# Optimization experiments

Hardware: AMD Instinct MI355X
Metric: run time of the kernel (lower is better)

The kernel has to match this reference:

```python
import jax, jax.numpy as jnp
import numpy as np

EPS = 1e-5

def _ln(x, g, b):
    mu = jnp.mean(x, axis=-1, keepdims=True)
    var = jnp.mean(jnp.square(x - mu), axis=-1, keepdims=True)
    return (x - mu) * jax.lax.rsqrt(var + EPS) * g + b

def setup_inputs() -> dict:
    key = jax.random.key(0)
    ks = jax.random.split(key, 16)
    B, L, D, H = 1, 512, 128, 128  # d_pair=128, d_hidden=128
    s_d = 1.0 / np.sqrt(D)
    s_h = 1.0 / np.sqrt(H)
    return {
        "pair": jax.random.normal(ks[0], (B, L, L, D), jnp.float32),
        "ln_g": jnp.ones((D,), jnp.float32),
        "ln_b": jnp.zeros((D,), jnp.float32),
        "lw": jax.random.normal(ks[1], (H, D), jnp.float32) * s_d,
        "lb": jnp.zeros((H,), jnp.float32),
        "lgw": jax.random.normal(ks[2], (H, D), jnp.float32) * s_d,
        "lgb": jnp.ones((H,), jnp.float32),
        "rw": jax.random.normal(ks[3], (H, D), jnp.float32) * s_d,
        "rb": jnp.zeros((H,), jnp.float32),
        "rgw": jax.random.normal(ks[4], (H, D), jnp.float32) * s_d,
        "rgb": jnp.ones((H,), jnp.float32),
        "gw": jax.random.normal(ks[5], (D, D), jnp.float32) * s_d,
        "gb": jnp.ones((D,), jnp.float32),
        "lno_g": jnp.ones((H,), jnp.float32),
        "lno_b": jnp.zeros((H,), jnp.float32),
        "ow": jax.random.normal(ks[6], (D, H), jnp.float32) * s_h,
        "ob": jnp.zeros((D,), jnp.float32),
    }

def reference(pair, ln_g, ln_b, lw, lb, lgw, lgb, rw, rb, rgw, rgb, gw, gb, lno_g, lno_b, ow, ob):
    L = pair.shape[1]
    p = _ln(pair, ln_g, ln_b)                                   # [B,L,L,D]
    left = jax.nn.sigmoid(p @ lgw.T + lgb) * (p @ lw.T + lb)    # [B,L,L,H]
    right = jax.nn.sigmoid(p @ rgw.T + rgb) * (p @ rw.T + rb)   # [B,L,L,H]
    # outgoing: contract over k (second seq dim)
    out = jnp.einsum('bikd,bjkd->bijd', left, right / jnp.float32(L))
    out = _ln(out, lno_g, lno_b)
    out = out @ ow.T + ob                                       # [B,L,L,D]
    gate = jax.nn.sigmoid(p @ gw.T + gb)
    return gate * out
```

## Files before the change

kernel.cpp:

```cpp
#include <hip/hip_runtime.h>
#include <hip/hip_bf16.h>
#include <stdint.h>

#define LSEQ 512
#define LL   262144

typedef __attribute__((ext_vector_type(8))) short short8;
typedef __attribute__((ext_vector_type(4))) float f32x4;
typedef __attribute__((ext_vector_type(4))) unsigned short us4;
typedef __attribute__((ext_vector_type(8))) unsigned short us8;

static_assert(sizeof(short8) == 16, "");
static_assert(sizeof(us8) == 16, "");

__device__ inline unsigned short f2bf(float f){
  unsigned u = __builtin_bit_cast(unsigned, f);
  unsigned r = (u + 0x7fffu + ((u >> 16) & 1u)) >> 16;
  return (unsigned short)r;
}
__device__ inline float bf2f(unsigned short s){
  return __builtin_bit_cast(float, ((unsigned)s) << 16);
}
__device__ inline float sigm(float x){ return 1.f / (1.f + __expf(-x)); }

__device__ inline int sw256(int row, int byte_in_row){
  return row*256 + ((((byte_in_row >> 4) ^ (row & 7))) << 4) + (byte_in_row & 15);
}
__device__ inline int sw128(int row, int byte_in_row){
  return row*128 + ((((byte_in_row >> 4) ^ (row & 7))) << 4) + (byte_in_row & 15);
}

__device__ inline void gload16(const void* g, void* lds){
  __builtin_amdgcn_global_load_lds(
      (const __attribute__((address_space(1))) unsigned*)g,
      (__attribute__((address_space(3))) unsigned*)lds, 16, 0, 0);
}

__global__ __launch_bounds__(128) void k0_prep(
    const float* __restrict__ ow, const float* __restrict__ lnog,
    const float* __restrict__ lnob, const float* __restrict__ ob,
    unsigned short* __restrict__ wgbf, float* __restrict__ swg, float* __restrict__ swb)
{
  const int dd = blockIdx.x;
  const int t  = threadIdx.x;
  const int idx = dd*128 + t;
  float o = ow[idx];
  float a = o * lnog[t];
  float b = o * lnob[t];
  wgbf[idx] = f2bf(a);
  #pragma unroll
  for (int m = 1; m < 64; m <<= 1){ a += __shfl_xor(a, m); b += __shfl_xor(b, m); }
  __shared__ float sA[2], sB[2];
  if ((t & 63) == 0){ sA[t >> 6] = a; sB[t >> 6] = b; }
  __syncthreads();
  if (t == 0){ swg[dd] = sA[0] + sA[1]; swb[dd] = sB[0] + sB[1] + ob[dd]; }
}

__global__ __launch_bounds__(64) void kP_pack(
    const float* __restrict__ lgw, const float* __restrict__ lw,
    const float* __restrict__ rgw, const float* __restrict__ rw,
    const float* __restrict__ gw, short8* __restrict__ wpk)
{
  const int b = blockIdx.x;
  const int arm = b >> 5, n = (b >> 2) & 7, ks = b & 3;
  const float* src = arm==0 ? lgw : arm==1 ? lw : arm==2 ? rgw : arm==3 ? rw : gw;
  const int l = threadIdx.x;
  const int h = n*16 + (l & 15), k0 = ks*32 + (l >> 4)*8;
  short8 v;
  #pragma unroll
  for (int e = 0; e < 8; ++e) v[e] = (short)f2bf(src[h*128 + k0 + e]);
  wpk[b*64 + l] = v;
}

__global__ __launch_bounds__(256, 3) void k1_proj(
    const float* __restrict__ pair, const float* __restrict__ ln_g, const float* __restrict__ ln_b,
    const float* __restrict__ lb,  const float* __restrict__ lgb,
    const float* __restrict__ rb,  const float* __restrict__ rgb,
    const float* __restrict__ gb,
    const short8* __restrict__ wpk,
    unsigned short* __restrict__ lt, unsigned short* __restrict__ rt,
    unsigned short* __restrict__ gate)
{
  __shared__ char p_l[16384];
  __shared__ char epi[16384];
  const int t = threadIdx.x;
  const int w = t >> 6, l = t & 63;
  const long pos0 = (long)blockIdx.x * 64;

  {
    const int col = (t & 31) * 4;
    const float4 g4 = *(const float4*)(ln_g + col);
    const float4 b4 = *(const float4*)(ln_b + col);
    #pragma unroll
    for (int pass = 0; pass < 8; ++pass){
      const int row = pass*8 + (t >> 5);
      const float4 x = *(const float4*)(pair + (pos0 + row)*128 + col);
      float s = x.x + x.y + x.z + x.w;
      float q = x.x*x.x + x.y*x.y + x.z*x.z + x.w*x.w;
      #pragma unroll
      for (int m = 1; m < 32; m <<= 1){ s += __shfl_xor(s, m); q += __shfl_xor(q, m); }
      const float mu = s * (1.f/128.f);
      const float rs = rsqrtf(q * (1.f/128.f) - mu*mu + 1e-5f);
      us4 o;
      o.x = f2bf((x.x - mu)*rs*g4.x + b4.x);
      o.y = f2bf((x.y - mu)*rs*g4.y + b4.y);
      o.z = f2bf((x.z - mu)*rs*g4.z + b4.z);
      o.w = f2bf((x.w - mu)*rs*g4.w + b4.w);
      *(us4*)(p_l + sw256(row, col*2)) = o;
    }
  }
  __syncthreads();

  short8 a[4][4];
  #pragma unroll
  for (int m = 0; m < 4; ++m)
    #pragma unroll
    for (int ks = 0; ks < 4; ++ks)
      a[m][ks] = *(const short8*)(p_l + sw256(m*16 + (l & 15), ks*64 + (l >> 4)*16));

  auto zero42 = [&](f32x4 (&acc)[4][2]){
    #pragma unroll
    for (int m = 0; m < 4; ++m){ acc[m][0] = f32x4{0,0,0,0}; acc[m][1] = f32x4{0,0,0,0}; }
  };

  auto gemm2 = [&](int armG, int armL, f32x4 (&aG)[4][2], f32x4 (&aL)[4][2]){
    #pragma unroll
    for (int n2 = 0; n2 < 2; ++n2){
      const int n = w*2 + n2;
      short8 bg[4], blv[4];
      #pragma unroll
      for (int ks = 0; ks < 4; ++ks){
        bg[ks]  = wpk[((armG*8 + n)*4 + ks)*64 + l];
        blv[ks] = wpk[((armL*8 + n)*4 + ks)*64 + l];
      }
      #pragma unroll
      for (int ks = 0; ks < 4; ++ks)
        #pragma unroll
        for (int m = 0; m < 4; ++m){
          aG[m][n2] = __builtin_amdgcn_mfma_f32_16x16x32_bf16(a[m][ks], bg[ks],  aG[m][n2], 0, 0, 0);
          aL[m][n2] = __builtin_amdgcn_mfma_f32_16x16x32_bf16(a[m][ks], blv[ks], aL[m][n2], 0, 0, 0);
        }
    }
  };

  auto epiT = [&](f32x4 (&aG)[4][2], f32x4 (&aL)[4][2],
                  const float* __restrict__ gbias, const float* __restrict__ lbias,
                  unsigned short* __restrict__ dst){
    #pragma unroll
    for (int n2 = 0; n2 < 2; ++n2){
      const int h = w*32 + n2*16 + (l & 15);
      const float gv = gbias[h], lv = lbias[h];
      #pragma unroll
      for (int m = 0; m < 4; ++m){
        us4 o;
        #pragma unroll
        for (int r = 0; r < 4; ++r)
          o[r] = f2bf(sigm(aG[m][n2][r] + gv) * (aL[m][n2][r] + lv));
        *(us4*)(epi + sw128(h, (m*16 + (l >> 4)*4)*2)) = o;
      }
    }
    __syncthreads();
    #pragma unroll
    for (int p = 0; p < 4; ++p){
      const int hh = p*32 + (t >> 3), ch = t & 7;
      us8 v = *(const us8*)(epi + sw128(hh, ch*16));
      *(us8*)(dst + (long)hh*LL + pos0 + ch*8) = v;
    }
    __syncthreads();
  };

  f32x4 aG[4][2], aL[4][2];

  zero42(aG); zero42(aL);
  gemm2(0, 1, aG, aL);
  epiT(aG, aL, lgb, lb, lt);

  zero42(aG); zero42(aL);
  gemm2(2, 3, aG, aL);
  epiT(aG, aL, rgb, rb, rt);

  zero42(aG);
  #pragma unroll
  for (int n2 = 0; n2 < 2; ++n2){
    const int n = w*2 + n2;
    short8 bg[4];
    #pragma unroll
    for (int ks = 0; ks < 4; ++ks) bg[ks] = wpk[((4*8 + n)*4 + ks)*64 + l];
    #pragma unroll
    for (int ks = 0; ks < 4; ++ks)
      #pragma unroll
      for (int m = 0; m < 4; ++m)
        aG[m][n2] = __builtin_amdgcn_mfma_f32_16x16x32_bf16(a[m][ks], bg[ks], aG[m][n2], 0, 0, 0);
  }
  {
    #pragma unroll
    for (int n2 = 0; n2 < 2; ++n2){
      const int h = w*32 + n2*16 + (l & 15);
      const float gv = gb[h];
      #pragma unroll
      for (int m = 0; m < 4; ++m)
        #pragma unroll
        for (int r = 0; r < 4; ++r){
          const int pos = m*16 + (l >> 4)*4 + r;
          *(unsigned short*)(epi + sw256(pos, h*2)) = f2bf(sigm(aG[m][n2][r] + gv));
        }
    }
    __syncthreads();
    #pragma unroll
    for (int p = 0; p < 4; ++p){
      const int row = p*16 + (t >> 4), ch = t & 15;
      us8 v = *(const us8*)(epi + sw256(row, ch*16));
      *(us8*)(gate + (pos0 + row)*128 + ch*8) = v;
    }
  }
}

__global__ __launch_bounds__(256) void k2_tri(
    const unsigned short* __restrict__ lt, const unsigned short* __restrict__ rt,
    unsigned short* __restrict__ omm)
{
  __shared__ char smem[32768];
  char* As = smem;
  char* Bs = smem + 16384;
  const int t = threadIdx.x, b = blockIdx.x;
  const int d = b & 127, tile = b >> 7;
  const int i0 = (tile >> 2)*128, j0 = (tile & 3)*128;
  const unsigned short* Ag = lt + (long)d*LL;
  const unsigned short* Bg = rt + (long)d*LL;
  const int w = t >> 6, l = t & 63;
  const int wm = w >> 1, wn = w & 1;

  f32x4 acc[4][4];
  #pragma unroll
  for (int m = 0; m < 4; ++m)
    #pragma unroll
    for (int n = 0; n < 4; ++n) acc[m][n] = f32x4{0.f,0.f,0.f,0.f};

  for (int kt = 0; kt < 8; ++kt){
    const int k0 = kt*64;
    __syncthreads();
    #pragma unroll
    for (int q = 0; q < 4; ++q){
      int P = q*4096 + t*16;
      int row = P >> 7;
      int ls  = ((P >> 4) & 7) ^ (row & 7);
      gload16(Ag + (long)(i0 + row)*512 + k0 + ls*8, As + P);
      gload16(Bg + (long)(j0 + row)*512 + k0 + ls*8, Bs + P);
    }
    __syncthreads();
    #pragma unroll
    for (int ks = 0; ks < 2; ++ks){
      short8 a[4], bb[4];
      #pragma unroll
      for (int m = 0; m < 4; ++m){
        int row = wm*64 + m*16 + (l & 15);
        a[m] = *(const short8*)(As + sw128(row, ks*64 + (l >> 4)*16));
      }
      #pragma unroll
      for (int n = 0; n < 4; ++n){
        int row = wn*64 + n*16 + (l & 15);
        bb[n] = *(const short8*)(Bs + sw128(row, ks*64 + (l >> 4)*16));
      }
      #pragma unroll
      for (int m = 0; m < 4; ++m)
        #pragma unroll
        for (int n = 0; n < 4; ++n)
          acc[m][n] = __builtin_amdgcn_mfma_f32_16x16x32_bf16(a[m], bb[n], acc[m][n], 0, 0, 0);
    }
  }
  __syncthreads();
  #pragma unroll
  for (int m = 0; m < 4; ++m)
    #pragma unroll
    for (int n = 0; n < 4; ++n)
      #pragma unroll
      for (int r = 0; r < 4; ++r){
        int row = wm*64 + m*16 + (l >> 4)*4 + r;
        int j   = wn*64 + n*16 + (l & 15);
        *(unsigned short*)(smem + sw256(row, j*2)) = f2bf(acc[m][n][r] * (1.f/512.f));
      }
  __syncthreads();
  #pragma unroll
  for (int it = 0; it < 8; ++it){
    int row = it*16 + (t >> 4), ch = t & 15;
    us8 v = *(const us8*)(smem + sw256(row, ch*16));
    *(us8*)(omm + (long)d*LL + (long)(i0 + row)*512 + j0 + ch*8) = v;
  }
}

__global__ __launch_bounds__(256) void k3_out(
    const unsigned short* __restrict__ omm, const unsigned short* __restrict__ gate,
    const unsigned short* __restrict__ wgbf,
    const float* __restrict__ swg, const float* __restrict__ swb,
    float* __restrict__ out)
{
  __shared__ char omm_l[32768];
  __shared__ char wg_l[32768];
  __shared__ float mu_s[128], rs_s[128];
  const int t = threadIdx.x;
  const int jt = blockIdx.x, i = blockIdx.y;
  const int j0 = jt*128;
  const int w = t >> 6, l = t & 63;

  {
    const int jc = t & 15, dg = t >> 4;
    float sum[8], sq[8];
    #pragma unroll
    for (int e = 0; e < 8; ++e){ sum[e] = 0.f; sq[e] = 0.f; }
    #pragma unroll
    for (int q = 0; q < 8; ++q){
      int dd = dg + q*16;
      us8 v = *(const us8*)(omm + (long)dd*LL + (long)i*512 + j0 + jc*8);
      *(us8*)(omm_l + dd*256 + jc*16) = v;
      #pragma unroll
      for (int e = 0; e < 8; ++e){
        float f = bf2f(v[e]);
        sum[e] += f; sq[e] += f*f;
      }
    }
    float* scr = (float*)wg_l;
    #pragma unroll
    for (int e = 0; e < 8; ++e){
      scr[dg*128 + jc*8 + e]        = sum[e];
      scr[2048 + dg*128 + jc*8 + e] = sq[e];
    }
  }
  __syncthreads();
  if (t < 128){
    const float* scr = (const float*)wg_l;
    float s1 = 0.f, s2 = 0.f;
    #pragma unroll
    for (int g = 0; g < 16; ++g){ s1 += scr[g*128 + t]; s2 += scr[2048 + g*128 + t]; }
    float mu = s1 * (1.f/128.f);
    float var = s2 * (1.f/128.f) - mu*mu;
    mu_s[t] = mu;
    rs_s[t] = rsqrtf(var + 1e-5f);
  }
  __syncthreads();
  #pragma unroll
  for (int q = 0; q < 8; ++q){
    int P = q*4096 + t*16;
    gload16((const char*)wgbf + sw256(P >> 8, P & 255), wg_l + P);
  }
  __syncthreads();

  f32x4 acc[2][8];
  #pragma unroll
  for (int m = 0; m < 2; ++m)
    #pragma unroll
    for (int n = 0; n < 8; ++n) acc[m][n] = f32x4{0.f,0.f,0.f,0.f};

  #pragma unroll
  for (int ks = 0; ks < 4; ++ks){
    short8 a[2];
    #pragma unroll
    for (int m = 0; m < 2; ++m){
      const int jj = w*32 + m*16 + (l & 15);
      short8 av;
      #pragma unroll
      for (int e = 0; e < 8; ++e){
        int dd = ks*32 + (l >> 4)*8 + e;
        av[e] = *(const short*)(omm_l + dd*256 + jj*2);
      }
      a[m] = av;
    }
    #pragma unroll
    for (int n = 0; n < 8; ++n){
      int row = n*16 + (l & 15);
      short8 bb = *(const short8*)(wg_l + sw256(row, ks*64 + (l >> 4)*16));
      #pragma unroll
      for (int m = 0; m < 2; ++m)
        acc[m][n] = __builtin_amdgcn_mfma_f32_16x16x32_bf16(a[m], bb, acc[m][n], 0, 0, 0);
    }
  }

  float swgv[8], swbv[8];
  #pragma unroll
  for (int n = 0; n < 8; ++n){ swgv[n] = swg[n*16 + (l & 15)]; swbv[n] = swb[n*16 + (l & 15)]; }
  #pragma unroll
  for (int m = 0; m < 2; ++m){
    #pragma unroll
    for (int r = 0; r < 4; ++r){
      int j = w*32 + m*16 + (l >> 4)*4 + r;
      float mu = mu_s[j], rs = rs_s[j];
      long rowoff = ((long)i*512 + j0 + j)*128;
      #pragma unroll
      for (int n = 0; n < 8; ++n){
        int ddx = n*16 + (l & 15);
        float val = rs*(acc[m][n][r] - mu*swgv[n]) + swbv[n];
        out[rowoff + ddx] = val * bf2f(gate[rowoff + ddx]);
      }
    }
  }
}

extern "C" void kernel_launch(void* const* d_in, const int* in_sizes, int n_in,
                              void* d_out, int out_size, void* d_ws, size_t ws_size,
                              hipStream_t stream)
{
  const float* pair = (const float*)d_in[0];
  const float* ln_g = (const float*)d_in[1];
  const float* ln_b = (const float*)d_in[2];
  const float* lw   = (const float*)d_in[3];
  const float* lb   = (const float*)d_in[4];
  const float* lgw  = (const float*)d_in[5];
  const float* lgb  = (const float*)d_in[6];
  const float* rw   = (const float*)d_in[7];
  const float* rb   = (const float*)d_in[8];
  const float* rgw  = (const float*)d_in[9];
  const float* rgb  = (const float*)d_in[10];
  const float* gw   = (const float*)d_in[11];
  const float* gb   = (const float*)d_in[12];
  const float* lnog = (const float*)d_in[13];
  const float* lnob = (const float*)d_in[14];
  const float* ow   = (const float*)d_in[15];
  const float* ob   = (const float*)d_in[16];
  float* out = (float*)d_out;

  char* ws = (char*)d_ws;
  unsigned short* lt   = (unsigned short*)(ws);
  unsigned short* rt   = (unsigned short*)(ws + (1l << 26));
  unsigned short* gate = (unsigned short*)(ws + (2l << 26));
  unsigned short* omm  = (unsigned short*)(ws + (3l << 26));
  short8*         wpk  = (short8*)(ws + (3l << 26));
  unsigned short* wgbf = (unsigned short*)(ws + (4l << 26));
  float* swg = (float*)(ws + (4l << 26) + 65536);
  float* swb = swg + 128;

  k0_prep<<<dim3(128), dim3(128), 0, stream>>>(ow, lnog, lnob, ob, wgbf, swg, swb);
  kP_pack<<<dim3(160), dim3(64), 0, stream>>>(lgw, lw, rgw, rw, gw, wpk);
  k1_proj<<<dim3(4096), dim3(256), 0, stream>>>(pair, ln_g, ln_b, lb, lgb, rb, rgb, gb,
                                                wpk, lt, rt, gate);
  k2_tri<<<dim3(2048), dim3(256), 0, stream>>>(lt, rt, omm);
  k3_out<<<dim3(4, 512), dim3(256), 0, stream>>>(omm, gate, wgbf, swg, swb, out);
}
```

Measured before the change: 297.9 us.

## Cut k1 LDS and registers, write lt/rt directly, remap k2 block order

The projection kernel drops its second 16KB LDS epilogue buffer and the preloaded A-fragment register array. It now reloads A fragments from LDS per k-step and writes the transposed lt/rt outputs straight from the MFMA accumulators as 8-byte stores, which removes two barriers per arm. Launch bounds rise to 4 blocks per CU, and the LayerNorm prologue loads four float4 per thread with a shorter shuffle reduction. The triangle kernel remaps block indices so consecutive blocks share the same d channel, probably to spread work across XCDs and reuse lt/rt in L2. The cost is more LDS reads and less coalesced global stores for lt/rt.

```diff
diff --git a/kernel.cpp b/kernel.cpp
--- a/kernel.cpp
+++ b/kernel.cpp
@@ -72,7 +72,7 @@
   wpk[b*64 + l] = v;
 }
 
-__global__ __launch_bounds__(256, 3) void k1_proj(
+__global__ __launch_bounds__(256, 4) void k1_proj(
     const float* __restrict__ pair, const float* __restrict__ ln_g, const float* __restrict__ ln_b,
     const float* __restrict__ lb,  const float* __restrict__ lgb,
     const float* __restrict__ rb,  const float* __restrict__ rgb,
@@ -82,70 +82,75 @@
     unsigned short* __restrict__ gate)
 {
   __shared__ char p_l[16384];
-  __shared__ char epi[16384];
   const int t = threadIdx.x;
   const int w = t >> 6, l = t & 63;
   const long pos0 = (long)blockIdx.x * 64;
 
   {
-    const int col = (t & 31) * 4;
-    const float4 g4 = *(const float4*)(ln_g + col);
-    const float4 b4 = *(const float4*)(ln_b + col);
-    #pragma unroll
-    for (int pass = 0; pass < 8; ++pass){
-      const int row = pass*8 + (t >> 5);
-      const float4 x = *(const float4*)(pair + (pos0 + row)*128 + col);
-      float s = x.x + x.y + x.z + x.w;
-      float q = x.x*x.x + x.y*x.y + x.z*x.z + x.w*x.w;
-      #pragma unroll
-      for (int m = 1; m < 32; m <<= 1){ s += __shfl_xor(s, m); q += __shfl_xor(q, m); }
+    const int q8 = t & 7;
+    float4 g4[4], b4[4];
+    #pragma unroll
+    for (int i = 0; i < 4; ++i){
+      g4[i] = *(const float4*)(ln_g + q8*4 + i*32);
+      b4[i] = *(const float4*)(ln_b + q8*4 + i*32);
+    }
+    #pragma unroll
+    for (int pass = 0; pass < 2; ++pass){
+      const int row = pass*32 + (t >> 3);
+      float4 x[4];
+      #pragma unroll
+      for (int i = 0; i < 4; ++i)
+        x[i] = *(const float4*)(pair + (pos0 + row)*128 + q8*4 + i*32);
+      float s = 0.f, qq = 0.f;
+      #pragma unroll
+      for (int i = 0; i < 4; ++i){
+        s  += (x[i].x + x[i].y) + (x[i].z + x[i].w);
+        qq += (x[i].x*x[i].x + x[i].y*x[i].y) + (x[i].z*x[i].z + x[i].w*x[i].w);
+      }
+      #pragma unroll
+      for (int msk = 1; msk < 8; msk <<= 1){ s += __shfl_xor(s, msk); qq += __shfl_xor(qq, msk); }
       const float mu = s * (1.f/128.f);
-      const float rs = rsqrtf(q * (1.f/128.f) - mu*mu + 1e-5f);
-      us4 o;
-      o.x = f2bf((x.x - mu)*rs*g4.x + b4.x);
-      o.y = f2bf((x.y - mu)*rs*g4.y + b4.y);
-      o.z = f2bf((x.z - mu)*rs*g4.z + b4.z);
-      o.w = f2bf((x.w - mu)*rs*g4.w + b4.w);
-      *(us4*)(p_l + sw256(row, col*2)) = o;
-    }
-  }
-  __syncthreads();
-
-  short8 a[4][4];
-  #pragma unroll
-  for (int m = 0; m < 4; ++m)
-    #pragma unroll
-    for (int ks = 0; ks < 4; ++ks)
-      a[m][ks] = *(const short8*)(p_l + sw256(m*16 + (l & 15), ks*64 + (l >> 4)*16));
-
-  auto zero42 = [&](f32x4 (&acc)[4][2]){
+      const float rs = rsqrtf(qq * (1.f/128.f) - mu*mu + 1e-5f);
+      #pragma unroll
+      for (int i = 0; i < 4; ++i){
+        us4 o;
+        o.x = f2bf((x[i].x - mu)*rs*g4[i].x + b4[i].x);
+        o.y = f2bf((x[i].y - mu)*rs*g4[i].y + b4[i].y);
+        o.z = f2bf((x[i].z - mu)*rs*g4[i].z + b4[i].z);
+        o.w = f2bf((x[i].w - mu)*rs*g4[i].w + b4[i].w);
+        *(us4*)(p_l + sw256(row, q8*8 + i*64)) = o;
+      }
+    }
+  }
+  __syncthreads();
+
+  f32x4 aG[4][2], aL[4][2];
+  auto zero = [&](f32x4 (&acc)[4][2]){
     #pragma unroll
     for (int m = 0; m < 4; ++m){ acc[m][0] = f32x4{0,0,0,0}; acc[m][1] = f32x4{0,0,0,0}; }
   };
-
-  auto gemm2 = [&](int armG, int armL, f32x4 (&aG)[4][2], f32x4 (&aL)[4][2]){
-    #pragma unroll
-    for (int n2 = 0; n2 < 2; ++n2){
-      const int n = w*2 + n2;
-      short8 bg[4], blv[4];
-      #pragma unroll
-      for (int ks = 0; ks < 4; ++ks){
-        bg[ks]  = wpk[((armG*8 + n)*4 + ks)*64 + l];
-        blv[ks] = wpk[((armL*8 + n)*4 + ks)*64 + l];
-      }
-      #pragma unroll
-      for (int ks = 0; ks < 4; ++ks)
+  auto gemm2 = [&](int armG, int armL){
+    #pragma unroll
+    for (int ks = 0; ks < 4; ++ks){
+      short8 av[4];
+      #pragma unroll
+      for (int m = 0; m < 4; ++m)
+        av[m] = *(const short8*)(p_l + sw256(m*16 + (l & 15), ks*64 + (l >> 4)*16));
+      #pragma unroll
+      for (int n2 = 0; n2 < 2; ++n2){
+        const int n = w*2 + n2;
+        const short8 bg = wpk[((armG*8 + n)*4 + ks)*64 + l];
+        const short8 bl = wpk[((armL*8 + n)*4 + ks)*64 + l];
         #pragma unroll
         for (int m = 0; m < 4; ++m){
-          aG[m][n2] = __builtin_amdgcn_mfma_f32_16x16x32_bf16(a[m][ks], bg[ks],  aG[m][n2], 0, 0, 0);
-          aL[m][n2] = __builtin_amdgcn_mfma_f32_16x16x32_bf16(a[m][ks], blv[ks], aL[m][n2], 0, 0, 0);
+          aG[m][n2] = __builtin_amdgcn_mfma_f32_16x16x32_bf16(av[m], bg, aG[m][n2], 0, 0, 0);
+          aL[m][n2] = __builtin_amdgcn_mfma_f32_16x16x32_bf16(av[m], bl, aL[m][n2], 0, 0, 0);
         }
+      }
     }
   };
-
-  auto epiT = [&](f32x4 (&aG)[4][2], f32x4 (&aL)[4][2],
-                  const float* __restrict__ gbias, const float* __restrict__ lbias,
-                  unsigned short* __restrict__ dst){
+  auto epiDirect = [&](const float* __restrict__ gbias, const float* __restrict__ lbias,
+                       unsigned short* __restrict__ dst){
     #pragma unroll
     for (int n2 = 0; n2 < 2; ++n2){
       const int h = w*32 + n2*16 + (l & 15);
@@ -156,62 +161,49 @@
         #pragma unroll
         for (int r = 0; r < 4; ++r)
           o[r] = f2bf(sigm(aG[m][n2][r] + gv) * (aL[m][n2][r] + lv));
-        *(us4*)(epi + sw128(h, (m*16 + (l >> 4)*4)*2)) = o;
-      }
-    }
-    __syncthreads();
-    #pragma unroll
-    for (int p = 0; p < 4; ++p){
-      const int hh = p*32 + (t >> 3), ch = t & 7;
-      us8 v = *(const us8*)(epi + sw128(hh, ch*16));
-      *(us8*)(dst + (long)hh*LL + pos0 + ch*8) = v;
-    }
-    __syncthreads();
+        *(us4*)(dst + (long)h*LL + pos0 + m*16 + (l >> 4)*4) = o;
+      }
+    }
   };
 
-  f32x4 aG[4][2], aL[4][2];
-
-  zero42(aG); zero42(aL);
-  gemm2(0, 1, aG, aL);
-  epiT(aG, aL, lgb, lb, lt);
-
-  zero42(aG); zero42(aL);
-  gemm2(2, 3, aG, aL);
-  epiT(aG, aL, rgb, rb, rt);
-
-  zero42(aG);
+  zero(aG); zero(aL); gemm2(0, 1); epiDirect(lgb, lb, lt);
+  zero(aG); zero(aL); gemm2(2, 3); epiDirect(rgb, rb, rt);
+
+  zero(aG);
+  #pragma unroll
+  for (int ks = 0; ks < 4; ++ks){
+    short8 av[4];
+    #pragma unroll
+    for (int m = 0; m < 4; ++m)
+      av[m] = *(const short8*)(p_l + sw256(m*16 + (l & 15), ks*64 + (l >> 4)*16));
+    #pragma unroll
+    for (int n2 = 0; n2 < 2; ++n2){
+      const int n = w*2 + n2;
+      const short8 bg = wpk[((4*8 + n)*4 + ks)*64 + l];
+      #pragma unroll
+      for (int m = 0; m < 4; ++m)
+        aG[m][n2] = __builtin_amdgcn_mfma_f32_16x16x32_bf16(av[m], bg, aG[m][n2], 0, 0, 0);
+    }
+  }
+  __syncthreads();
   #pragma unroll
   for (int n2 = 0; n2 < 2; ++n2){
-    const int n = w*2 + n2;
-    short8 bg[4];
-    #pragma unroll
-    for (int ks = 0; ks < 4; ++ks) bg[ks] = wpk[((4*8 + n)*4 + ks)*64 + l];
-    #pragma unroll
-    for (int ks = 0; ks < 4; ++ks)
-      #pragma unroll
-      for (int m = 0; m < 4; ++m)
-        aG[m][n2] = __builtin_amdgcn_mfma_f32_16x16x32_bf16(a[m][ks], bg[ks], aG[m][n2], 0, 0, 0);
-  }
-  {
-    #pragma unroll
-    for (int n2 = 0; n2 < 2; ++n2){
-      const int h = w*32 + n2*16 + (l & 15);
-      const float gv = gb[h];
-      #pragma unroll
-      for (int m = 0; m < 4; ++m)
-        #pragma unroll
-        for (int r = 0; r < 4; ++r){
-          const int pos = m*16 + (l >> 4)*4 + r;
-          *(unsigned short*)(epi + sw256(pos, h*2)) = f2bf(sigm(aG[m][n2][r] + gv));
-        }
-    }
-    __syncthreads();
-    #pragma unroll
-    for (int p = 0; p < 4; ++p){
-      const int row = p*16 + (t >> 4), ch = t & 15;
-      us8 v = *(const us8*)(epi + sw256(row, ch*16));
-      *(us8*)(gate + (pos0 + row)*128 + ch*8) = v;
-    }
+    const int h = w*32 + n2*16 + (l & 15);
+    const float gv = gb[h];
+    #pragma unroll
+    for (int m = 0; m < 4; ++m)
+      #pragma unroll
+      for (int r = 0; r < 4; ++r){
+        const int pos = m*16 + (l >> 4)*4 + r;
+        *(unsigned short*)(p_l + sw256(pos, h*2)) = f2bf(sigm(aG[m][n2][r] + gv));
+      }
+  }
+  __syncthreads();
+  #pragma unroll
+  for (int p = 0; p < 4; ++p){
+    const int row = p*16 + (t >> 4), ch = t & 15;
+    us8 v = *(const us8*)(p_l + sw256(row, ch*16));
+    *(us8*)(gate + (pos0 + row)*128 + ch*8) = v;
   }
 }
 
@@ -222,8 +214,10 @@
   __shared__ char smem[32768];
   char* As = smem;
   char* Bs = smem + 16384;
-  const int t = threadIdx.x, b = blockIdx.x;
-  const int d = b & 127, tile = b >> 7;
+  const int t = threadIdx.x;
+  const int b0 = blockIdx.x;
+  const int b  = (b0 & 7) * 256 + (b0 >> 3);
+  const int d = b >> 4, tile = b & 15;
   const int i0 = (tile >> 2)*128, j0 = (tile & 3)*128;
   const unsigned short* Ag = lt + (long)d*LL;
   const unsigned short* Bg = rt + (long)d*LL;
```

Result: slower. 338.3 us (+13.6%).
